# Optimization experiments

Measured on AMD Instinct MI355X. Metric: run time of the kernel, lower is better.

## Reference

```python
import jax, jax.numpy as jnp
import numpy as np

F_IN = 512
F_OUT = 512
HEADS = 8  # all heads share the same weights in the original module
NEG_SLOPE = 0.01  # nn.LeakyReLU default
MASK_VAL = -1.0e10


def setup_inputs() -> dict:
    key = jax.random.key(0)
    ks = jax.random.split(key, 6)
    B, N = 8, 2048
    X_input = jax.random.normal(ks[0], (B, N, F_IN), dtype=jnp.float32)
    u = jax.random.uniform(ks[1], (B, N, N), dtype=jnp.float32)
    A_input = jnp.maximum((u < 0.02).astype(jnp.float32), jnp.eye(N, dtype=jnp.float32)[None])
    # learned params (nn.Linear stores W as [out,in]; we use [in,out] with x @ W)
    Wk = jax.random.normal(ks[2], (F_IN, F_OUT), dtype=jnp.float32) / np.sqrt(F_IN).astype(np.float32)
    bk = jnp.zeros((F_OUT,), dtype=jnp.float32)
    ws = jax.random.normal(ks[3], (F_OUT,), dtype=jnp.float32) / np.sqrt(F_OUT).astype(np.float32)
    bs = jnp.zeros((), dtype=jnp.float32)
    wn = jax.random.normal(ks[4], (F_OUT,), dtype=jnp.float32) / np.sqrt(F_OUT).astype(np.float32)
    bn = jnp.zeros((), dtype=jnp.float32)
    return {"X_input": X_input, "A_input": A_input, "Wk": Wk, "bk": bk,
            "ws": ws, "bs": bs, "wn": wn, "bn": bn}


def reference(X_input, A_input, Wk, bk, ws, bs, wn, bn):
    # shared projection (identical across all heads in the original loop)
    feat = jnp.einsum('bnf,fg->bng', X_input, Wk) + bk          # [B,N,F_]
    a_self = jnp.einsum('bng,g->bn', feat, ws) + bs             # [B,N]
    a_neigh = jnp.einsum('bng,g->bn', feat, wn) + bn            # [B,N]
    # torch.bmm([B,N,1],[B,1,N]) -> multiplicative outer product score
    att = jax.nn.leaky_relu(a_self[:, :, None] * a_neigh[:, None, :], NEG_SLOPE)
    att = att + MASK_VAL * (1.0 - A_input)                      # [B,N,N]
    p = jax.nn.softmax(att, axis=-1)
    nf = jnp.einsum('bij,bjg->big', p, feat)                    # [B,N,F_]
    # concat of HEADS identical head outputs, then tanh
    out = jnp.tanh(jnp.concatenate([nf] * HEADS, axis=-1))      # [B,N,HEADS*F_]
    return out
```

## Files before the change

kernel.cpp:

```cpp
#include <hip/hip_runtime.h>

#define NEG_SLOPE 0.01f
#define B_ 8
#define N_ 2048
#define F_ 512

typedef unsigned short u16;
typedef __attribute__((ext_vector_type(8))) unsigned short u16x8;
typedef __attribute__((ext_vector_type(8))) _Float16 f16x8;
typedef __attribute__((ext_vector_type(4))) float f32x4;

__device__ __forceinline__ f32x4 mfma16f(u16x8 a, u16x8 b, f32x4 c) {
    return __builtin_amdgcn_mfma_f32_16x16x32_f16(
        __builtin_bit_cast(f16x8, a), __builtin_bit_cast(f16x8, b), c, 0, 0, 0);
}

__device__ __forceinline__ void load_lds16(const void* g, void* l) {
    __builtin_amdgcn_global_load_lds(
        (__attribute__((address_space(1))) void*)(void*)g,
        (__attribute__((address_space(3))) void*)l, 16, 0, 0);
}

__global__ __launch_bounds__(256) void prep_all(const float* __restrict__ Wk,
                                                const float* __restrict__ bk,
                                                const float* __restrict__ ws,
                                                const float* __restrict__ bs,
                                                const float* __restrict__ wn,
                                                const float* __restrict__ bn,
                                                u16* __restrict__ Wf,
                                                float* __restrict__ ws2,
                                                float* __restrict__ wn2,
                                                float* __restrict__ csn) {
    const int bid = blockIdx.x, t = threadIdx.x;
    if (bid < 1024) {
        const int id = bid * 256 + t;
        const int k = id & 511, n = id >> 9;
        ((_Float16*)Wf)[id] = (_Float16)Wk[k * 512 + n];
        return;
    }
    const int lane = t & 63, w = t >> 6;
    if (bid >= 1280) {
        if (w == 0) {
            const int sel = bid - 1280;
            const float* vec = sel ? wn : ws;
            const float4 b0 = *(const float4*)(bk + lane * 8);
            const float4 b1 = *(const float4*)(bk + lane * 8 + 4);
            const float4 v0 = *(const float4*)(vec + lane * 8);
            const float4 v1 = *(const float4*)(vec + lane * 8 + 4);
            float d = b0.x * v0.x + b0.y * v0.y + b0.z * v0.z + b0.w * v0.w +
                      b1.x * v1.x + b1.y * v1.y + b1.z * v1.z + b1.w * v1.w;
#pragma unroll
            for (int m = 32; m; m >>= 1) d += __shfl_xor(d, m);
            if (lane == 0) csn[sel] = d + (sel ? bn[0] : bs[0]);
        }
        return;
    }
    const int W = (bid - 1024) * 4 + w;
    const int k = W & 511;
    const float* vec = (W < 512) ? ws : wn;
    const float4 w0 = *(const float4*)(Wk + (size_t)k * 512 + lane * 8);
    const float4 w1 = *(const float4*)(Wk + (size_t)k * 512 + lane * 8 + 4);
    const float4 v0 = *(const float4*)(vec + lane * 8);
    const float4 v1 = *(const float4*)(vec + lane * 8 + 4);
    float d = w0.x * v0.x + w0.y * v0.y + w0.z * v0.z + w0.w * v0.w +
              w1.x * v1.x + w1.y * v1.y + w1.z * v1.z + w1.w * v1.w;
#pragma unroll
    for (int m = 32; m; m >>= 1) d += __shfl_xor(d, m);
    if (lane == 0) ((W < 512) ? ws2 : wn2)[k] = d;
}

__global__ __launch_bounds__(256) void gemm_feat(const float* __restrict__ X,
                                                 const u16* __restrict__ Wf,
                                                 const float* __restrict__ bk,
                                                 u16* __restrict__ feat) {
    __shared__ u16 Af[128 * 64];
    __shared__ u16 Bf[128 * 64];
    const int t = threadIdx.x;
    const int lane = t & 63;
    const int w = t >> 6;
    const int bid = blockIdx.x;
    const int tm = (bid & 7) * 16 + (bid >> 5);
    const int tn = (bid >> 3) & 3;
    const int wr = w >> 1, wc = w & 1;

    f32x4 acc[4][4];
#pragma unroll
    for (int m = 0; m < 4; ++m)
#pragma unroll
        for (int n = 0; n < 4; ++n) acc[m][n] = {0.f, 0.f, 0.f, 0.f};

    const int lrow = lane >> 3;
    const int scol = ((lane & 7) ^ lrow) * 8;
    const u16* Bbase = Wf + ((size_t)(tn * 128 + w * 8 + lrow)) * 512 + scol;
    u16* BfW = Bf + (w * 8) * 64;

    const int arow = t >> 3;
    const int akk = (t & 7) * 8;
    const float* Abase = X + ((size_t)(tm * 128 + arow)) * 512 + akk;
    u16* AfW = Af + arow * 64 + (akk ^ ((arow & 7) * 8));

    for (int k0 = 0; k0 < 512; k0 += 64) {
#pragma unroll
        for (int iss = 0; iss < 4; ++iss)
            load_lds16(Bbase + (size_t)(iss * 32) * 512 + k0, BfW + iss * 32 * 64);
#pragma unroll
        for (int p = 0; p < 4; ++p) {
            const float4 x0 = *(const float4*)(Abase + (size_t)(p * 32) * 512 + k0);
            const float4 x1 = *(const float4*)(Abase + (size_t)(p * 32) * 512 + k0 + 4);
            const float xv[8] = {x0.x, x0.y, x0.z, x0.w, x1.x, x1.y, x1.z, x1.w};
            u16x8 hv;
#pragma unroll
            for (int e = 0; e < 8; ++e)
                hv[e] = __builtin_bit_cast(u16, (_Float16)xv[e]);
            *(u16x8*)(AfW + p * 32 * 64) = hv;
        }
        __syncthreads();
        const int swz = (lane & 7) * 8;
#pragma unroll
        for (int kk = 0; kk < 64; kk += 32) {
            u16x8 af[4], bf[4];
            const int aoff = (kk + (lane >> 4) * 8) ^ swz;
#pragma unroll
            for (int m = 0; m < 4; ++m)
                af[m] = *(const u16x8*)(Af + (wr * 64 + m * 16 + (lane & 15)) * 64 + aoff);
#pragma unroll
            for (int n = 0; n < 4; ++n)
                bf[n] = *(const u16x8*)(Bf + (wc * 64 + n * 16 + (lane & 15)) * 64 + aoff);
#pragma unroll
            for (int m = 0; m < 4; ++m)
#pragma unroll
                for (int n = 0; n < 4; ++n)
                    acc[m][n] = mfma16f(af[m], bf[n], acc[m][n]);
        }
        __syncthreads();
    }

    const int crow0 = tm * 128 + wr * 64;
    const int ccol0 = tn * 128 + wc * 64;
    _Float16* feat16 = (_Float16*)feat;
#pragma unroll
    for (int n = 0; n < 4; ++n) {
        const int gc = ccol0 + n * 16 + (lane & 15);
        const float bkv = bk[gc];
#pragma unroll
        for (int m = 0; m < 4; ++m) {
            const int gr = crow0 + m * 16 + (lane >> 4) * 4;
#pragma unroll
            for (int r = 0; r < 4; ++r)
                feat16[(size_t)(gr + r) * 512 + gc] = (_Float16)(acc[m][n][r] + bkv);
        }
    }
}

__global__ __launch_bounds__(256) void dots_x(const float* __restrict__ X,
                                              const float* __restrict__ ws2,
                                              const float* __restrict__ wn2,
                                              const float* __restrict__ csn,
                                              float* __restrict__ a_self,
                                              float* __restrict__ a_neigh) {
    const int t = threadIdx.x, lane = t & 63, w = t >> 6;
    const int row = blockIdx.x * 4 + w;
    const float4 f0 = *(const float4*)(X + (size_t)row * 512 + lane * 8);
    const float4 f1 = *(const float4*)(X + (size_t)row * 512 + lane * 8 + 4);
    const float fv[8] = {f0.x, f0.y, f0.z, f0.w, f1.x, f1.y, f1.z, f1.w};
    const float4 sa = *(const float4*)(ws2 + lane * 8);
    const float4 sb = *(const float4*)(ws2 + lane * 8 + 4);
    const float4 na = *(const float4*)(wn2 + lane * 8);
    const float4 nb = *(const float4*)(wn2 + lane * 8 + 4);
    float ds = fv[0] * sa.x + fv[1] * sa.y + fv[2] * sa.z + fv[3] * sa.w +
               fv[4] * sb.x + fv[5] * sb.y + fv[6] * sb.z + fv[7] * sb.w;
    float dn = fv[0] * na.x + fv[1] * na.y + fv[2] * na.z + fv[3] * na.w +
               fv[4] * nb.x + fv[5] * nb.y + fv[6] * nb.z + fv[7] * nb.w;
#pragma unroll
    for (int m = 32; m; m >>= 1) {
        ds += __shfl_xor(ds, m);
        dn += __shfl_xor(dn, m);
    }
    if (lane == 0) {
        a_self[row] = ds + csn[0];
        a_neigh[row] = dn + csn[1];
    }
}

__global__ __launch_bounds__(256) void attn_row(const float* __restrict__ A,
                                                const u16* __restrict__ feat,
                                                const float* __restrict__ a_self,
                                                const float* __restrict__ a_neigh,
                                                float* __restrict__ out) {
    const int bid = blockIdx.x;
    const int t = threadIdx.x;
    const int lane = t & 63, w = t >> 6;
    const int b = bid & 7;
    const int row = b * N_ + (bid >> 3) * 4 + w;

    const float asi = a_self[row];
    const float4* Arow4 = (const float4*)(A + (size_t)row * N_);
    const float4* An4   = (const float4*)(a_neigh + (size_t)b * N_);

    float sv[32];
    unsigned selbits = 0;
    float mloc = -3.0e38f;
#pragma unroll
    for (int c = 0; c < 8; ++c) {
        const float4 a  = Arow4[c * 64 + lane];
        const float4 an = An4[c * 64 + lane];
        const float avi[4] = {a.x, a.y, a.z, a.w};
        const float ani[4] = {an.x, an.y, an.z, an.w};
#pragma unroll
        for (int i = 0; i < 4; ++i) {
            float s = asi * ani[i];
            s = s > 0.f ? s : NEG_SLOPE * s;
            sv[c * 4 + i] = s;
            if (avi[i] != 0.f) {
                selbits |= 1u << (c * 4 + i);
                mloc = fmaxf(mloc, s);
            }
        }
    }
    float mx = mloc;
#pragma unroll
    for (int m = 32; m; m >>= 1) mx = fmaxf(mx, __shfl_xor(mx, m));

    const u16* frow = feat + (size_t)b * N_ * F_ + lane * 8;
    float acc[8] = {0.f, 0.f, 0.f, 0.f, 0.f, 0.f, 0.f, 0.f};
    float ssum = 0.f;
#pragma unroll
    for (int e = 0; e < 32; ++e) {
        unsigned long long mask = __ballot((selbits >> e) & 1u);
        while (mask) {
            const int l = __builtin_ctzll(mask);
            mask &= mask - 1;
            const float s = __shfl(sv[e], l);
            const float p = __expf(s - mx);
            const int j = (e >> 2) * 256 + l * 4 + (e & 3);
            const f16x8 vv = *(const f16x8*)(frow + (size_t)j * F_);
#pragma unroll
            for (int i = 0; i < 8; ++i) acc[i] += p * (float)vv[i];
            ssum += p;
        }
    }
    const float inv = 1.f / ssum;

    float o[8];
#pragma unroll
    for (int i = 0; i < 8; ++i) o[i] = tanhf(acc[i] * inv);
    const float4 o0 = {o[0], o[1], o[2], o[3]};
    const float4 o1 = {o[4], o[5], o[6], o[7]};
    float* obase = out + (size_t)row * (8 * F_) + lane * 8;
#pragma unroll
    for (int h = 0; h < 8; ++h) {
        *(float4*)(obase + h * F_)     = o0;
        *(float4*)(obase + h * F_ + 4) = o1;
    }
}

extern "C" void kernel_launch(void* const* d_in, const int* in_sizes, int n_in,
                              void* d_out, int out_size, void* d_ws, size_t ws_size,
                              hipStream_t stream) {
    const float* X  = (const float*)d_in[0];
    const float* A  = (const float*)d_in[1];
    const float* Wk = (const float*)d_in[2];
    const float* bk = (const float*)d_in[3];
    const float* ws = (const float*)d_in[4];
    const float* bs = (const float*)d_in[5];
    const float* wn = (const float*)d_in[6];
    const float* bn = (const float*)d_in[7];
    float* out = (float*)d_out;

    char* wsb = (char*)d_ws;
    u16*   feat    = (u16*)(wsb);
    u16*   Wf      = (u16*)(wsb + 16777216);
    float* a_self  = (float*)(wsb + 17301504);
    float* a_neigh = (float*)(wsb + 17367040);
    float* ws2     = (float*)(wsb + 17432576);
    float* wn2     = (float*)(wsb + 17434624);
    float* csn     = (float*)(wsb + 17436672);

    prep_all   <<<dim3(1282),  dim3(256), 0, stream>>>(Wk, bk, ws, bs, wn, bn, Wf, ws2, wn2, csn);
    dots_x     <<<dim3(4096),  dim3(256), 0, stream>>>(X, ws2, wn2, csn, a_self, a_neigh);
    gemm_feat  <<<dim3(512),   dim3(256), 0, stream>>>(X, Wf, bk, feat);
    attn_row   <<<dim3(4096),  dim3(256), 0, stream>>>(A, feat, a_self, a_neigh, out);
}
```

Baseline: 160.5 us.

## Split attention into a neighbor-compaction kernel and a gather-accumulate kernel

The attention kernel is split in two. A compaction pass scans each adjacency row, computes normalized softmax weights and writes a compact list of (weight, column) pairs plus a count per row. A separate gather pass walks that list with a 4-way unrolled loop, so it avoids the per-element ballot/shuffle/exp work and can issue more feature loads at once. The cost is an extra launch and a round trip of the list through global memory. The list is capped at 128 entries per row; at about 2% density (around 41 expected neighbors) this should rarely overflow, but an overflowing row would write past its slot.

New measurement: 155.8 us. -2.9%, faster.

```diff
diff --git a/kernel.cpp b/kernel.cpp
--- a/kernel.cpp
+++ b/kernel.cpp
@@ -182,16 +182,15 @@
     }
 }
 
-__global__ __launch_bounds__(256) void attn_row(const float* __restrict__ A,
-                                                const u16* __restrict__ feat,
-                                                const float* __restrict__ a_self,
-                                                const float* __restrict__ a_neigh,
-                                                float* __restrict__ out) {
+__global__ __launch_bounds__(256) void compact_rows(const float* __restrict__ A,
+                                                    const float* __restrict__ a_self,
+                                                    const float* __restrict__ a_neigh,
+                                                    float2* __restrict__ list,
+                                                    int* __restrict__ cnt_arr) {
     const int bid = blockIdx.x;
-    const int t = threadIdx.x;
-    const int lane = t & 63, w = t >> 6;
-    const int b = bid & 7;
-    const int row = b * N_ + (bid >> 3) * 4 + w;
+    const int t = threadIdx.x, lane = t & 63, w = t >> 6;
+    const int row = bid * 4 + w;
+    const int b = row >> 11;
 
     const float asi = a_self[row];
     const float4* Arow4 = (const float4*)(A + (size_t)row * N_);
@@ -221,29 +220,94 @@
 #pragma unroll
     for (int m = 32; m; m >>= 1) mx = fmaxf(mx, __shfl_xor(mx, m));
 
+    float lsum = 0.f;
+    {
+        unsigned mbits = selbits;
+        while (mbits) {
+            const int e = __builtin_ctz(mbits);
+            mbits &= mbits - 1;
+            const float p = __expf(sv[e] - mx);
+            sv[e] = p;
+            lsum += p;
+        }
+    }
+    float tot = lsum;
+#pragma unroll
+    for (int m = 32; m; m >>= 1) tot += __shfl_xor(tot, m);
+    const float inv = 1.f / tot;
+
+    const int cntl = __popc(selbits);
+    int v = cntl;
+#pragma unroll
+    for (int off = 1; off < 64; off <<= 1) {
+        const int u = __shfl_up(v, off);
+        if (lane >= off) v += u;
+    }
+    if (lane == 63) cnt_arr[row] = v;
+    int pos = v - cntl;
+
+    float2* lr = list + (size_t)row * 128;
+    {
+        unsigned mbits = selbits;
+        while (mbits) {
+            const int e = __builtin_ctz(mbits);
+            mbits &= mbits - 1;
+            const int j = (e >> 2) * 256 + lane * 4 + (e & 3);
+            lr[pos] = make_float2(sv[e] * inv, (float)j);
+            ++pos;
+        }
+    }
+}
+
+__global__ __launch_bounds__(256) void gather_rows(const float2* __restrict__ list,
+                                                   const int* __restrict__ cnt_arr,
+                                                   const u16* __restrict__ feat,
+                                                   float* __restrict__ out) {
+    const int bid = blockIdx.x;
+    const int t = threadIdx.x, lane = t & 63, w = t >> 6;
+    const int b = bid & 7;
+    const int row = b * N_ + (bid >> 3) * 4 + w;
+
+    const int cnt = cnt_arr[row];
+    const float2* lr = list + (size_t)row * 128;
+    const float2 e0 = lr[lane];
+    const float2 e1 = lr[64 + lane];
+
     const u16* frow = feat + (size_t)b * N_ * F_ + lane * 8;
     float acc[8] = {0.f, 0.f, 0.f, 0.f, 0.f, 0.f, 0.f, 0.f};
-    float ssum = 0.f;
-#pragma unroll
-    for (int e = 0; e < 32; ++e) {
-        unsigned long long mask = __ballot((selbits >> e) & 1u);
-        while (mask) {
-            const int l = __builtin_ctzll(mask);
-            mask &= mask - 1;
-            const float s = __shfl(sv[e], l);
-            const float p = __expf(s - mx);
-            const int j = (e >> 2) * 256 + l * 4 + (e & 3);
-            const f16x8 vv = *(const f16x8*)(frow + (size_t)j * F_);
-#pragma unroll
-            for (int i = 0; i < 8; ++i) acc[i] += p * (float)vv[i];
-            ssum += p;
-        }
-    }
-    const float inv = 1.f / ssum;
+
+    const int c0 = cnt < 64 ? cnt : 64;
+    int k = 0;
+    for (; k + 4 <= c0; k += 4) {
+        const float p0 = __shfl(e0.x, k),     j0 = __shfl(e0.y, k);
+        const float p1 = __shfl(e0.x, k + 1), j1 = __shfl(e0.y, k + 1);
+        const float p2 = __shfl(e0.x, k + 2), j2 = __shfl(e0.y, k + 2);
+        const float p3 = __shfl(e0.x, k + 3), j3 = __shfl(e0.y, k + 3);
+        const f16x8 v0 = *(const f16x8*)(frow + (size_t)(int)j0 * F_);
+        const f16x8 v1 = *(const f16x8*)(frow + (size_t)(int)j1 * F_);
+        const f16x8 v2 = *(const f16x8*)(frow + (size_t)(int)j2 * F_);
+        const f16x8 v3 = *(const f16x8*)(frow + (size_t)(int)j3 * F_);
+#pragma unroll
+        for (int i = 0; i < 8; ++i)
+            acc[i] += (p0 * (float)v0[i] + p1 * (float)v1[i]) +
+                      (p2 * (float)v2[i] + p3 * (float)v3[i]);
+    }
+    for (; k < c0; ++k) {
+        const float p0 = __shfl(e0.x, k), j0 = __shfl(e0.y, k);
+        const f16x8 v0 = *(const f16x8*)(frow + (size_t)(int)j0 * F_);
+#pragma unroll
+        for (int i = 0; i < 8; ++i) acc[i] += p0 * (float)v0[i];
+    }
+    for (k = 64; k < cnt; ++k) {
+        const float p0 = __shfl(e1.x, k - 64), j0 = __shfl(e1.y, k - 64);
+        const f16x8 v0 = *(const f16x8*)(frow + (size_t)(int)j0 * F_);
+#pragma unroll
+        for (int i = 0; i < 8; ++i) acc[i] += p0 * (float)v0[i];
+    }
 
     float o[8];
 #pragma unroll
-    for (int i = 0; i < 8; ++i) o[i] = tanhf(acc[i] * inv);
+    for (int i = 0; i < 8; ++i) o[i] = tanhf(acc[i]);
     const float4 o0 = {o[0], o[1], o[2], o[3]};
     const float4 o1 = {o[4], o[5], o[6], o[7]};
     float* obase = out + (size_t)row * (8 * F_) + lane * 8;
@@ -275,9 +339,12 @@
     float* ws2     = (float*)(wsb + 17432576);
     float* wn2     = (float*)(wsb + 17434624);
     float* csn     = (float*)(wsb + 17436672);
-
-    prep_all   <<<dim3(1282),  dim3(256), 0, stream>>>(Wk, bk, ws, bs, wn, bn, Wf, ws2, wn2, csn);
-    dots_x     <<<dim3(4096),  dim3(256), 0, stream>>>(X, ws2, wn2, csn, a_self, a_neigh);
-    gemm_feat  <<<dim3(512),   dim3(256), 0, stream>>>(X, Wf, bk, feat);
-    attn_row   <<<dim3(4096),  dim3(256), 0, stream>>>(A, feat, a_self, a_neigh, out);
-}
+    int*   cnt_arr = (int*)(wsb + 17440768);
+    float2* list   = (float2*)(wsb + 17825792);
+
+    prep_all     <<<dim3(1282), dim3(256), 0, stream>>>(Wk, bk, ws, bs, wn, bn, Wf, ws2, wn2, csn);
+    dots_x       <<<dim3(4096), dim3(256), 0, stream>>>(X, ws2, wn2, csn, a_self, a_neigh);
+    compact_rows <<<dim3(4096), dim3(256), 0, stream>>>(A, a_self, a_neigh, list, cnt_arr);
+    gemm_feat    <<<dim3(512),  dim3(256), 0, stream>>>(X, Wf, bk, feat);
+    gather_rows  <<<dim3(4096), dim3(256), 0, stream>>>(list, cnt_arr, feat, out);
+}
```

## Replace sparse per-row attention gather with dense MFMA attention over transposed features

Applied to the files above, without the earlier changes.

The per-row sparse gather kernel is replaced by a dense tiled kernel. It computes masked softmax weights for every column, packs them to fp16 and multiplies them with a transposed feature matrix using MFMA. Instead of a row max, a per-batch upper bound on the score is built from global min/max of a_neigh (tracked with atomics), so no second pass is needed. The GEMM now writes features transposed, and the weight transpose in prep is flipped. This trades wasted dense FLOPs on a 2%-dense mask for regular, coalesced access and tensor-core throughput. The bound-based offset risks fp16 underflow or overflow of the weights.

Result: slower. 329.5 us (+105.3%).

```diff
diff --git a/kernel.cpp b/kernel.cpp
--- a/kernel.cpp
+++ b/kernel.cpp
@@ -6,8 +6,12 @@
 #define F_ 512
 
 typedef unsigned short u16;
+typedef unsigned int u32;
 typedef __attribute__((ext_vector_type(8))) unsigned short u16x8;
+typedef __attribute__((ext_vector_type(4))) unsigned short u16x4;
+typedef __attribute__((ext_vector_type(4))) unsigned int u32x4;
 typedef __attribute__((ext_vector_type(8))) _Float16 f16x8;
+typedef __attribute__((ext_vector_type(2))) _Float16 f16x2;
 typedef __attribute__((ext_vector_type(4))) float f32x4;
 
 __device__ __forceinline__ f32x4 mfma16f(u16x8 a, u16x8 b, f32x4 c) {
@@ -19,6 +23,15 @@
     __builtin_amdgcn_global_load_lds(
         (__attribute__((address_space(1))) void*)(void*)g,
         (__attribute__((address_space(3))) void*)l, 16, 0, 0);
+}
+
+__device__ __forceinline__ u32 fkey(float f) {
+    const u32 u = __float_as_uint(f);
+    return (u & 0x80000000u) ? ~u : (u | 0x80000000u);
+}
+__device__ __forceinline__ float fdec(u32 k) {
+    return (k & 0x80000000u) ? __uint_as_float(k & 0x7FFFFFFFu)
+                             : __uint_as_float(~k);
 }
 
 __global__ __launch_bounds__(256) void prep_all(const float* __restrict__ Wk,
@@ -30,15 +43,20 @@
                                                 u16* __restrict__ Wf,
                                                 float* __restrict__ ws2,
                                                 float* __restrict__ wn2,
-                                                float* __restrict__ csn) {
+                                                float* __restrict__ csn,
+                                                u32* __restrict__ anmm) {
     const int bid = blockIdx.x, t = threadIdx.x;
     if (bid < 1024) {
         const int id = bid * 256 + t;
-        const int k = id & 511, n = id >> 9;
-        ((_Float16*)Wf)[id] = (_Float16)Wk[k * 512 + n];
+        const int k = id >> 9, n = id & 511;
+        ((_Float16*)Wf)[(size_t)n * 512 + k] = (_Float16)Wk[id];
         return;
     }
     const int lane = t & 63, w = t >> 6;
+    if (bid == 1282) {
+        if (t < 16) anmm[t] = (t & 1) ? 0xFFFFFFFFu : 0u;
+        return;
+    }
     if (bid >= 1280) {
         if (w == 0) {
             const int sel = bid - 1280;
@@ -72,7 +90,7 @@
 __global__ __launch_bounds__(256) void gemm_feat(const float* __restrict__ X,
                                                  const u16* __restrict__ Wf,
                                                  const float* __restrict__ bk,
-                                                 u16* __restrict__ feat) {
+                                                 u16* __restrict__ featT) {
     __shared__ u16 Af[128 * 64];
     __shared__ u16 Bf[128 * 64];
     const int t = threadIdx.x;
@@ -137,7 +155,6 @@
 
     const int crow0 = tm * 128 + wr * 64;
     const int ccol0 = tn * 128 + wc * 64;
-    _Float16* feat16 = (_Float16*)feat;
 #pragma unroll
     for (int n = 0; n < 4; ++n) {
         const int gc = ccol0 + n * 16 + (lane & 15);
@@ -145,9 +162,12 @@
 #pragma unroll
         for (int m = 0; m < 4; ++m) {
             const int gr = crow0 + m * 16 + (lane >> 4) * 4;
+            const int b = gr >> 11, j = gr & 2047;
+            u16x4 pk;
 #pragma unroll
             for (int r = 0; r < 4; ++r)
-                feat16[(size_t)(gr + r) * 512 + gc] = (_Float16)(acc[m][n][r] + bkv);
+                pk[r] = __builtin_bit_cast(u16, (_Float16)(acc[m][n][r] + bkv));
+            *(u16x4*)(featT + ((size_t)(b * 512 + gc)) * 2048 + j) = pk;
         }
     }
 }
@@ -157,7 +177,9 @@
                                               const float* __restrict__ wn2,
                                               const float* __restrict__ csn,
                                               float* __restrict__ a_self,
-                                              float* __restrict__ a_neigh) {
+                                              float* __restrict__ a_neigh,
+                                              u32* __restrict__ anmm) {
+    __shared__ float redn[4];
     const int t = threadIdx.x, lane = t & 63, w = t >> 6;
     const int row = blockIdx.x * 4 + w;
     const float4 f0 = *(const float4*)(X + (size_t)row * 512 + lane * 8);
@@ -176,81 +198,157 @@
         ds += __shfl_xor(ds, m);
         dn += __shfl_xor(dn, m);
     }
+    const float dnf = dn + csn[1];
     if (lane == 0) {
         a_self[row] = ds + csn[0];
-        a_neigh[row] = dn + csn[1];
-    }
-}
-
-__global__ __launch_bounds__(256) void attn_row(const float* __restrict__ A,
-                                                const u16* __restrict__ feat,
-                                                const float* __restrict__ a_self,
-                                                const float* __restrict__ a_neigh,
-                                                float* __restrict__ out) {
+        a_neigh[row] = dnf;
+        redn[w] = dnf;
+    }
+    __syncthreads();
+    if (t == 0) {
+        const float mx = fmaxf(fmaxf(redn[0], redn[1]), fmaxf(redn[2], redn[3]));
+        const float mn = fminf(fminf(redn[0], redn[1]), fminf(redn[2], redn[3]));
+        const int b = row >> 11;
+        atomicMax(&anmm[b * 2], fkey(mx));
+        atomicMin(&anmm[b * 2 + 1], fkey(mn));
+    }
+}
+
+__global__ __launch_bounds__(256) void attn_dense(const float* __restrict__ A,
+                                                  const u16* __restrict__ featT,
+                                                  const float* __restrict__ a_self,
+                                                  const float* __restrict__ a_neigh,
+                                                  const u32* __restrict__ anmm,
+                                                  float* __restrict__ out) {
+    __shared__ float an_lds[N_];
+    __shared__ u16 bt[1024 * 8];
     const int bid = blockIdx.x;
-    const int t = threadIdx.x;
-    const int lane = t & 63, w = t >> 6;
     const int b = bid & 7;
-    const int row = b * N_ + (bid >> 3) * 4 + w;
-
-    const float asi = a_self[row];
-    const float4* Arow4 = (const float4*)(A + (size_t)row * N_);
-    const float4* An4   = (const float4*)(a_neigh + (size_t)b * N_);
-
-    float sv[32];
-    unsigned selbits = 0;
-    float mloc = -3.0e38f;
-#pragma unroll
-    for (int c = 0; c < 8; ++c) {
-        const float4 a  = Arow4[c * 64 + lane];
-        const float4 an = An4[c * 64 + lane];
-        const float avi[4] = {a.x, a.y, a.z, a.w};
-        const float ani[4] = {an.x, an.y, an.z, an.w};
-#pragma unroll
-        for (int i = 0; i < 4; ++i) {
-            float s = asi * ani[i];
-            s = s > 0.f ? s : NEG_SLOPE * s;
-            sv[c * 4 + i] = s;
-            if (avi[i] != 0.f) {
-                selbits |= 1u << (c * 4 + i);
-                mloc = fmaxf(mloc, s);
+    const int mt = (bid >> 3) & 31;
+    const int nt = bid >> 8;
+    const int t = threadIdx.x, lane = t & 63, w = t >> 6;
+    const int mq = w >> 1, nh = w & 1;
+    const int mR = mt * 64 + mq * 32;
+    const int nC = nt * 256 + nh * 128;
+
+    {
+        const f32x4* src = (const f32x4*)(a_neigh + (size_t)b * N_);
+        ((f32x4*)an_lds)[t] = src[t];
+        ((f32x4*)an_lds)[256 + t] = src[256 + t];
+    }
+
+    const float asi0 = a_self[(size_t)b * N_ + mR + (lane & 15)];
+    const float asi1 = a_self[(size_t)b * N_ + mR + 16 + (lane & 15)];
+    const float anmax = fdec(anmm[b * 2]);
+    const float anmin = fdec(anmm[b * 2 + 1]);
+    float um0 = asi0 > 0.f ? asi0 * anmax : asi0 * anmin;
+    um0 = fmaxf(um0, 0.01f * um0);
+    float um1 = asi1 > 0.f ? asi1 * anmax : asi1 * anmin;
+    um1 = fmaxf(um1, 0.01f * um1);
+    const float uoff0 = um0 - 7.f, uoff1 = um1 - 7.f;
+
+    const float* A0 = A + ((size_t)b * N_ + mR + (lane & 15)) * N_ + (lane >> 4) * 8;
+    const float* A1 = A0 + (size_t)16 * N_;
+
+    int slotn[4], csrc[4];
+#pragma unroll
+    for (int i = 0; i < 4; ++i) {
+        const int slot = i * 256 + t;
+        slotn[i] = slot >> 2;
+        csrc[i] = (slot & 3) ^ ((slotn[i] >> 1) & 3);
+    }
+    const u16* ftb = featT + (size_t)(b * 512 + nt * 256) * 2048;
+
+    f32x4 acc[2][8];
+#pragma unroll
+    for (int ma = 0; ma < 2; ++ma)
+#pragma unroll
+        for (int nf = 0; nf < 8; ++nf) acc[ma][nf] = {0.f, 0.f, 0.f, 0.f};
+    float ssum0 = 0.f, ssum1 = 0.f;
+    const int bbyte = (((lane >> 4) ^ (((lane & 15) >> 1) & 3)) * 16);
+    const char* btb = (const char*)bt + (nh * 128 + (lane & 15)) * 64 + bbyte;
+
+    for (int k0 = 0; k0 < N_; k0 += 32) {
+#pragma unroll
+        for (int i = 0; i < 4; ++i)
+            load_lds16(ftb + (size_t)slotn[i] * 2048 + k0 + csrc[i] * 8,
+                       (char*)bt + (i * 256 + w * 64) * 16);
+        const f32x4 a0a = __builtin_nontemporal_load((const f32x4*)(A0 + k0));
+        const f32x4 a0b = __builtin_nontemporal_load((const f32x4*)(A0 + k0 + 4));
+        const f32x4 a1a = __builtin_nontemporal_load((const f32x4*)(A1 + k0));
+        const f32x4 a1b = __builtin_nontemporal_load((const f32x4*)(A1 + k0 + 4));
+        __syncthreads();
+
+        const f32x4 anA = *(const f32x4*)&an_lds[k0 + (lane >> 4) * 8];
+        const f32x4 anB = *(const f32x4*)&an_lds[k0 + (lane >> 4) * 8 + 4];
+        const float anv[8] = {anA.x, anA.y, anA.z, anA.w, anB.x, anB.y, anB.z, anB.w};
+        const float av0[8] = {a0a.x, a0a.y, a0a.z, a0a.w, a0b.x, a0b.y, a0b.z, a0b.w};
+        const float av1[8] = {a1a.x, a1a.y, a1a.z, a1a.w, a1b.x, a1b.y, a1b.z, a1b.w};
+
+        float p0[8], p1[8];
+#pragma unroll
+        for (int e = 0; e < 8; ++e) {
+            float s = asi0 * anv[e];
+            s = fmaxf(s, 0.01f * s);
+            float p = __expf(s - uoff0);
+            p = (av0[e] != 0.f) ? p : 0.f;
+            ssum0 += p;
+            p0[e] = p;
+        }
+#pragma unroll
+        for (int e = 0; e < 8; ++e) {
+            float s = asi1 * anv[e];
+            s = fmaxf(s, 0.01f * s);
+            float p = __expf(s - uoff1);
+            p = (av1[e] != 0.f) ? p : 0.f;
+            ssum1 += p;
+            p1[e] = p;
+        }
+        u32x4 w0, w1;
+#pragma unroll
+        for (int e2 = 0; e2 < 4; ++e2) {
+            w0[e2] = __builtin_bit_cast(u32,
+                __builtin_amdgcn_cvt_pkrtz(p0[2 * e2], p0[2 * e2 + 1]));
+            w1[e2] = __builtin_bit_cast(u32,
+                __builtin_amdgcn_cvt_pkrtz(p1[2 * e2], p1[2 * e2 + 1]));
+        }
+        const u16x8 P0 = __builtin_bit_cast(u16x8, w0);
+        const u16x8 P1 = __builtin_bit_cast(u16x8, w1);
+
+#pragma unroll
+        for (int nf = 0; nf < 8; ++nf) {
+            const u16x8 bf = *(const u16x8*)(btb + nf * 1024);
+            acc[0][nf] = mfma16f(P0, bf, acc[0][nf]);
+            acc[1][nf] = mfma16f(P1, bf, acc[1][nf]);
+        }
+        __syncthreads();
+    }
+
+    ssum0 += __shfl_xor(ssum0, 16); ssum0 += __shfl_xor(ssum0, 32);
+    ssum1 += __shfl_xor(ssum1, 16); ssum1 += __shfl_xor(ssum1, 32);
+    float inv0[4], inv1[4];
+#pragma unroll
+    for (int r = 0; r < 4; ++r) {
+        inv0[r] = 1.f / __shfl(ssum0, (lane >> 4) * 4 + r);
+        inv1[r] = 1.f / __shfl(ssum1, (lane >> 4) * 4 + r);
+    }
+
+#pragma unroll
+    for (int ma = 0; ma < 2; ++ma) {
+        const int rowg = b * N_ + mR + ma * 16 + (lane >> 4) * 4;
+#pragma unroll
+        for (int nf = 0; nf < 8; ++nf) {
+            const int col = nC + nf * 16 + (lane & 15);
+#pragma unroll
+            for (int r = 0; r < 4; ++r) {
+                const float iv = ma ? inv1[r] : inv0[r];
+                const float val = tanhf(acc[ma][nf][r] * iv);
+                float* p = out + (size_t)(rowg + r) * (8 * F_) + col;
+#pragma unroll
+                for (int h = 0; h < 8; ++h)
+                    __builtin_nontemporal_store(val, p + h * F_);
             }
         }
-    }
-    float mx = mloc;
-#pragma unroll
-    for (int m = 32; m; m >>= 1) mx = fmaxf(mx, __shfl_xor(mx, m));
-
-    const u16* frow = feat + (size_t)b * N_ * F_ + lane * 8;
-    float acc[8] = {0.f, 0.f, 0.f, 0.f, 0.f, 0.f, 0.f, 0.f};
-    float ssum = 0.f;
-#pragma unroll
-    for (int e = 0; e < 32; ++e) {
-        unsigned long long mask = __ballot((selbits >> e) & 1u);
-        while (mask) {
-            const int l = __builtin_ctzll(mask);
-            mask &= mask - 1;
-            const float s = __shfl(sv[e], l);
-            const float p = __expf(s - mx);
-            const int j = (e >> 2) * 256 + l * 4 + (e & 3);
-            const f16x8 vv = *(const f16x8*)(frow + (size_t)j * F_);
-#pragma unroll
-            for (int i = 0; i < 8; ++i) acc[i] += p * (float)vv[i];
-            ssum += p;
-        }
-    }
-    const float inv = 1.f / ssum;
-
-    float o[8];
-#pragma unroll
-    for (int i = 0; i < 8; ++i) o[i] = tanhf(acc[i] * inv);
-    const float4 o0 = {o[0], o[1], o[2], o[3]};
-    const float4 o1 = {o[4], o[5], o[6], o[7]};
-    float* obase = out + (size_t)row * (8 * F_) + lane * 8;
-#pragma unroll
-    for (int h = 0; h < 8; ++h) {
-        *(float4*)(obase + h * F_)     = o0;
-        *(float4*)(obase + h * F_ + 4) = o1;
     }
 }
 
@@ -268,16 +366,17 @@
     float* out = (float*)d_out;
 
     char* wsb = (char*)d_ws;
-    u16*   feat    = (u16*)(wsb);
+    u16*   featT   = (u16*)(wsb);
     u16*   Wf      = (u16*)(wsb + 16777216);
     float* a_self  = (float*)(wsb + 17301504);
     float* a_neigh = (float*)(wsb + 17367040);
     float* ws2     = (float*)(wsb + 17432576);
     float* wn2     = (float*)(wsb + 17434624);
     float* csn     = (float*)(wsb + 17436672);
-
-    prep_all   <<<dim3(1282),  dim3(256), 0, stream>>>(Wk, bk, ws, bs, wn, bn, Wf, ws2, wn2, csn);
-    dots_x     <<<dim3(4096),  dim3(256), 0, stream>>>(X, ws2, wn2, csn, a_self, a_neigh);
-    gemm_feat  <<<dim3(512),   dim3(256), 0, stream>>>(X, Wf, bk, feat);
-    attn_row   <<<dim3(4096),  dim3(256), 0, stream>>>(A, feat, a_self, a_neigh, out);
-}
+    u32*   anmm    = (u32*)(wsb + 17440768);
+
+    prep_all   <<<dim3(1283), dim3(256), 0, stream>>>(Wk, bk, ws, bs, wn, bn, Wf, ws2, wn2, csn, anmm);
+    dots_x     <<<dim3(4096), dim3(256), 0, stream>>>(X, ws2, wn2, csn, a_self, a_neigh, anmm);
+    gemm_feat  <<<dim3(512),  dim3(256), 0, stream>>>(X, Wf, bk, featT);
+    attn_dense <<<dim3(512),  dim3(256), 0, stream>>>(A, featT, a_self, a_neigh, anmm, out);
+}
```
